# Optimization experiments

Measured on AMD Instinct MI355X. Metric: run time of the kernel, lower is better.

## Reference

```python
import jax, jax.numpy as jnp
import numpy as np

N = 10000
E = 160000
D_IN = 512
D_OUT = 512


def setup_inputs() -> dict:
    key = jax.random.key(0)
    k1, k2, k3, k4, k5 = jax.random.split(key, 5)
    x = jax.random.normal(k1, (N, D_IN), dtype=jnp.float32)
    edge_index = jax.random.randint(k2, (2, E), 0, N, dtype=jnp.int64)
    edge_attr = jax.random.uniform(k3, (E,), dtype=jnp.float32)
    W = jax.random.normal(k4, (D_IN, D_OUT), dtype=jnp.float32) * 0.05
    b = jax.random.normal(k5, (D_OUT,), dtype=jnp.float32) * 0.05
    return {"x": x, "edge_index": edge_index, "edge_attr": edge_attr, "W": W, "b": b}


def reference(x, edge_index, edge_attr, W, b):
    # PyG GCNConv with normalize=True, add_self_loops=True, edge_weight=edge_attr.
    n = x.shape[0]
    row, col = edge_index[0], edge_index[1]
    # Add self loops with weight 1.0 (fill_value=1.)
    loop = jnp.arange(n, dtype=edge_index.dtype)
    row_f = jnp.concatenate([row, loop])      # [E+N] source nodes
    col_f = jnp.concatenate([col, loop])      # [E+N] target nodes
    ew = jnp.concatenate([edge_attr, jnp.ones((n,), dtype=edge_attr.dtype)])
    # Symmetric normalization: deg computed over target index (col)
    deg = jax.ops.segment_sum(ew, col_f, num_segments=n)
    dinv = jnp.where(deg > 0, jax.lax.rsqrt(deg), 0.0)
    norm = dinv[row_f] * ew * dinv[col_f]     # [E+N]
    # Linear transform (no bias inside lin), then gather-scale-scatter
    h = x @ W                                  # [N, D_OUT]
    msg = h[row_f] * norm[:, None]             # [E+N, D_OUT]
    out = jax.ops.segment_sum(msg, col_f, num_segments=n)
    return out + b
```

## Files before the change

### kernel.cpp

```cpp
#include <hip/hip_runtime.h>

#define NN 10000
#define EE 160000
#define DD 512
#define CAP 128

typedef float floatx4 __attribute__((ext_vector_type(4)));
typedef short short8 __attribute__((ext_vector_type(8)));

#define AS3(p) ((__attribute__((address_space(3))) void*)(p))
#define AS1(p) ((const __attribute__((address_space(1))) void*)(p))

static __device__ __forceinline__ unsigned short f2bf(float f) {
    unsigned int u = __float_as_uint(f);
    unsigned int r = (u + 0x7fffu + ((u >> 16) & 1u)) >> 16;
    return (unsigned short)r;
}
static __device__ __forceinline__ unsigned int cvtpk(float a, float b) {
    unsigned int r;
    asm("v_cvt_pk_bf16_f32 %0, %1, %2" : "=v"(r) : "v"(a), "v"(b));
    return r;
}
static __device__ __forceinline__ float bflo(unsigned int u) {
    return __uint_as_float(u << 16);
}
static __device__ __forceinline__ float bfhi(unsigned int u) {
    return __uint_as_float(u & 0xffff0000u);
}


#define XB_BLOCKS 5000
#define WT_BLOCKS 256
#define ZERO_BLOCKS 20
#define EDGE_BLOCKS 625
#define GM_BLOCKS (157 * 4)

__global__ __launch_bounds__(256) void k_prep_xw(const float* __restrict__ x,
                                                 const float* __restrict__ W,
                                                 unsigned short* __restrict__ xb,
                                                 unsigned short* __restrict__ wtb,
                                                 uint4* __restrict__ zbase) {
    const int b = blockIdx.x;
    const int tid = threadIdx.x;
    if (b < XB_BLOCKS) {
        int gid = b * 256 + tid;
        float4 v = *(const float4*)&x[(size_t)gid * 4];
        *(uint2*)&xb[(size_t)gid * 4] = make_uint2(cvtpk(v.x, v.y), cvtpk(v.z, v.w));
    } else if (b < XB_BLOCKS + WT_BLOCKS) {
        __shared__ float T[32][33];
        int idx = b - XB_BLOCKS;
        int bi = idx & 15;
        int bj = idx >> 4;
        int r0 = tid >> 5;
        int cc = tid & 31;
        #pragma unroll
        for (int k = 0; k < 4; k++) {
            int r = r0 + k * 8;
            T[r][cc] = W[(size_t)(bi * 32 + r) * DD + bj * 32 + cc];
        }
        __syncthreads();
        #pragma unroll
        for (int k = 0; k < 4; k++) {
            int r = r0 + k * 8;
            wtb[(size_t)(bj * 32 + r) * DD + bi * 32 + cc] = f2bf(T[cc][r]);
        }
    } else {
        int idx = (b - XB_BLOCKS - WT_BLOCKS) * 256 + tid;
        zbase[idx] = make_uint4(0u, 0u, 0u, 0u);
    }
}


__global__ __launch_bounds__(256) void k_gemm_edge(const unsigned short* __restrict__ xb,
                                                   const unsigned short* __restrict__ wtb,
                                                   unsigned short* __restrict__ hb,
                                                   const int* __restrict__ row,
                                                   const int* __restrict__ col,
                                                   const float* __restrict__ ew,
                                                   float* __restrict__ deg,
                                                   int* __restrict__ cursor,
                                                   uint2* __restrict__ erw) {
    __shared__ unsigned short As[64 * 32];
    __shared__ unsigned short Bs[128 * 32];

    const int tid = threadIdx.x;

    if (blockIdx.x < EDGE_BLOCKS) {
        int e = blockIdx.x * 256 + tid;
        int r = row[e];
        int t = col[e];
        float w = ew[e];
        atomicAdd(&deg[t], w);
        int p = atomicAdd(&cursor[t], 1);
        if (p < CAP) erw[t * CAP + p] = make_uint2((unsigned int)r, __float_as_uint(w));
        return;
    }

    const int bid = blockIdx.x - EDGE_BLOCKS;
    const int wave = tid >> 6;
    const int lane = tid & 63;

    const int bm = (bid >> 2) * 64;
    const int bn = (bid & 3) * 128;

    const int wm = (wave >> 1) * 32;
    const int wn = (wave & 1) * 64;

    const int fm = lane & 15;
    const int kb = (lane >> 4) * 8;

    floatx4 acc[2][4];
    #pragma unroll
    for (int i = 0; i < 2; i++)
        #pragma unroll
        for (int j = 0; j < 4; j++)
            acc[i][j] = (floatx4){0.f, 0.f, 0.f, 0.f};

    const int srow = lane >> 2;
    const int scol = (lane & 3) * 8;

    for (int k0 = 0; k0 < DD; k0 += 32) {
        {
            int r = wave * 16 + srow;
            int gr = bm + r; if (gr > NN - 1) gr = NN - 1;
            __builtin_amdgcn_global_load_lds(AS1(xb + (size_t)gr * DD + k0 + scol),
                                             AS3(&As[wave * 512]), 16, 0, 0);
        }
        #pragma unroll
        for (int cc = 0; cc < 2; cc++) {
            int c = wave + cc * 4;
            int nr = bn + c * 16 + srow;
            __builtin_amdgcn_global_load_lds(AS1(wtb + (size_t)nr * DD + k0 + scol),
                                             AS3(&Bs[c * 512]), 16, 0, 0);
        }
        __syncthreads();

        short8 af[2], bfr[4];
        #pragma unroll
        for (int mi = 0; mi < 2; mi++)
            af[mi] = *(const short8*)&As[(wm + mi * 16 + fm) * 32 + kb];
        #pragma unroll
        for (int ni = 0; ni < 4; ni++)
            bfr[ni] = *(const short8*)&Bs[(wn + ni * 16 + fm) * 32 + kb];

        #pragma unroll
        for (int mi = 0; mi < 2; mi++)
            #pragma unroll
            for (int ni = 0; ni < 4; ni++)
                acc[mi][ni] = __builtin_amdgcn_mfma_f32_16x16x32_bf16(af[mi], bfr[ni], acc[mi][ni], 0, 0, 0);

        __syncthreads();
    }

    #pragma unroll
    for (int mi = 0; mi < 2; mi++) {
        #pragma unroll
        for (int ni = 0; ni < 4; ni++) {
            int colg = bn + wn + ni * 16 + (lane & 15);
            int rbase = bm + wm + mi * 16 + (lane >> 4) * 4;
            #pragma unroll
            for (int j = 0; j < 4; j++) {
                int rg = rbase + j;
                if (rg < NN) hb[(size_t)rg * DD + colg] = f2bf(acc[mi][ni][j]);
            }
        }
    }
}


#define EDGE_FMA(P, W) a0 += bflo(P) * W; a1 += bfhi(P) * W;

__global__ __launch_bounds__(128, 8) void k_aggregate(const int* __restrict__ cursor,
                                                      const uint2* __restrict__ erw,
                                                      const unsigned short* __restrict__ hb,
                                                      const float* __restrict__ deg,
                                                      const float* __restrict__ bias,
                                                      float* __restrict__ out) {
    const int h = threadIdx.x >> 6;
    const int t = threadIdx.x & 63;
    const int bid = blockIdx.x;
    const int q = bid & 3;
    const int i = (bid >> 2) * 2 + h;
    const int c = q * 128 + t * 2;

    __shared__ int   s_r[2][CAP];
    __shared__ float s_w[2][CAP];

    int cnt = cursor[i];
    if (cnt > CAP) cnt = CAP;
    const uint2* bkt = erw + (size_t)i * CAP;
    if (t < cnt) {
        uint2 p = bkt[t];
        int r = (int)p.x;
        s_r[h][t] = r << 9;
        s_w[h][t] = __uint_as_float(p.y) * rsqrtf(deg[r] + 1.0f);
    }
    if (t + 64 < cnt) {
        uint2 p = bkt[t + 64];
        int r = (int)p.x;
        s_r[h][t + 64] = r << 9;
        s_w[h][t + 64] = __uint_as_float(p.y) * rsqrtf(deg[r] + 1.0f);
    }

    float dv = rsqrtf(deg[i] + 1.0f);
    unsigned int hv = *(const unsigned int*)&hb[(size_t)i * DD + c];
    float2 bv = *(const float2*)&bias[c];

    __syncthreads();

    float a0 = 0.f, a1 = 0.f;

    int j = 0;
    for (; j + 8 <= cnt; j += 8) {
        unsigned int p0 = *(const unsigned int*)&hb[s_r[h][j    ] + c];
        unsigned int p1 = *(const unsigned int*)&hb[s_r[h][j + 1] + c];
        unsigned int p2 = *(const unsigned int*)&hb[s_r[h][j + 2] + c];
        unsigned int p3 = *(const unsigned int*)&hb[s_r[h][j + 3] + c];
        unsigned int p4 = *(const unsigned int*)&hb[s_r[h][j + 4] + c];
        unsigned int p5 = *(const unsigned int*)&hb[s_r[h][j + 5] + c];
        unsigned int p6 = *(const unsigned int*)&hb[s_r[h][j + 6] + c];
        unsigned int p7 = *(const unsigned int*)&hb[s_r[h][j + 7] + c];
        float w0 = s_w[h][j],     w1 = s_w[h][j + 1], w2 = s_w[h][j + 2], w3 = s_w[h][j + 3];
        float w4 = s_w[h][j + 4], w5 = s_w[h][j + 5], w6 = s_w[h][j + 6], w7 = s_w[h][j + 7];
        EDGE_FMA(p0, w0) EDGE_FMA(p1, w1) EDGE_FMA(p2, w2) EDGE_FMA(p3, w3)
        EDGE_FMA(p4, w4) EDGE_FMA(p5, w5) EDGE_FMA(p6, w6) EDGE_FMA(p7, w7)
    }
    for (; j + 4 <= cnt; j += 4) {
        unsigned int p0 = *(const unsigned int*)&hb[s_r[h][j    ] + c];
        unsigned int p1 = *(const unsigned int*)&hb[s_r[h][j + 1] + c];
        unsigned int p2 = *(const unsigned int*)&hb[s_r[h][j + 2] + c];
        unsigned int p3 = *(const unsigned int*)&hb[s_r[h][j + 3] + c];
        float w0 = s_w[h][j], w1 = s_w[h][j + 1], w2 = s_w[h][j + 2], w3 = s_w[h][j + 3];
        EDGE_FMA(p0, w0) EDGE_FMA(p1, w1) EDGE_FMA(p2, w2) EDGE_FMA(p3, w3)
    }
    for (; j < cnt; j++) {
        unsigned int p0 = *(const unsigned int*)&hb[s_r[h][j] + c];
        float w0 = s_w[h][j];
        EDGE_FMA(p0, w0)
    }

    float2 o;
    o.x = (a0 + bflo(hv) * dv) * dv + bv.x;
    o.y = (a1 + bfhi(hv) * dv) * dv + bv.y;
    *(float2*)&out[(size_t)i * DD + c] = o;
}

extern "C" void kernel_launch(void* const* d_in, const int* in_sizes, int n_in,
                              void* d_out, int out_size, void* d_ws, size_t ws_size,
                              hipStream_t stream) {
    const float* x  = (const float*)d_in[0];
    const int*   ei = (const int*)d_in[1];
    const float* ea = (const float*)d_in[2];
    const float* W  = (const float*)d_in[3];
    const float* b  = (const float*)d_in[4];
    float* out = (float*)d_out;

    char* ws = (char*)d_ws;
    unsigned short* hb   = (unsigned short*)ws;
    unsigned short* xb   = (unsigned short*)(ws + 10240000);
    unsigned short* wtb  = (unsigned short*)(ws + 20480000);
    float* deg    = (float*)(ws + 21004288);
    int*   cursor = (int*)  (ws + 21045248);
    uint2* erw    = (uint2*)(ws + 21086208);

    const int* row = ei;
    const int* col = ei + EE;

    k_prep_xw<<<XB_BLOCKS + WT_BLOCKS + ZERO_BLOCKS, 256, 0, stream>>>(x, W, xb, wtb, (uint4*)deg);

    k_gemm_edge<<<EDGE_BLOCKS + GM_BLOCKS, 256, 0, stream>>>(xb, wtb, hb, row, col, ea,
                                                             deg, cursor, erw);

    k_aggregate<<<NN * 2, 128, 0, stream>>>(cursor, erw, hb, deg, b, out);
}
```

Measured before the change: 128.5 us.

## Fuse three kernels into one persistent cooperative kernel with grid syncs

```diff
diff --git a/kernel.cpp b/kernel.cpp
--- a/kernel.cpp
+++ b/kernel.cpp
@@ -1,4 +1,5 @@
 #include <hip/hip_runtime.h>
+#include <hip/hip_cooperative_groups.h>
 
 #define NN 10000
 #define EE 160000
@@ -28,12 +29,193 @@
     return __uint_as_float(u & 0xffff0000u);
 }
 
-
-#define XB_BLOCKS 5000
-#define WT_BLOCKS 256
-#define ZERO_BLOCKS 20
-#define EDGE_BLOCKS 625
-#define GM_BLOCKS (157 * 4)
+#define XB_TASKS 5000
+#define WT_TASKS 256
+#define ZERO_TASKS 20
+#define PREP_TASKS (XB_TASKS + WT_TASKS + ZERO_TASKS)
+#define GEMM_TASKS 628
+#define EDGE_TASKS 625
+#define PHASEB_TASKS (GEMM_TASKS + EDGE_TASKS)
+#define AGG_TASKS (NN * 2)
+
+__global__ __launch_bounds__(256) void k_fused(const float* __restrict__ x,
+                                               const float* __restrict__ W,
+                                               const int* __restrict__ row,
+                                               const int* __restrict__ col,
+                                               const float* __restrict__ ew,
+                                               unsigned short* __restrict__ xb,
+                                               unsigned short* __restrict__ wtb,
+                                               unsigned short* __restrict__ hb,
+                                               float* __restrict__ deg,
+                                               int* __restrict__ cursor,
+                                               uint2* __restrict__ erw,
+                                               const float* __restrict__ bias,
+                                               float* __restrict__ out) {
+    __shared__ unsigned short As[64 * 32];
+    __shared__ unsigned short Bs[128 * 32];
+    __shared__ float T[32][33];
+
+    const int tid = threadIdx.x;
+    const int nb = gridDim.x;
+    const int wave = tid >> 6;
+    const int lane = tid & 63;
+
+    for (int task = blockIdx.x; task < PREP_TASKS; task += nb) {
+        if (task < XB_TASKS) {
+            int gid = task * 256 + tid;
+            float4 v = *(const float4*)&x[(size_t)gid * 4];
+            *(uint2*)&xb[(size_t)gid * 4] = make_uint2(cvtpk(v.x, v.y), cvtpk(v.z, v.w));
+        } else if (task < XB_TASKS + WT_TASKS) {
+            int idx = task - XB_TASKS;
+            int bi = idx & 15;
+            int bj = idx >> 4;
+            int r0 = tid >> 5;
+            int cc = tid & 31;
+            #pragma unroll
+            for (int k = 0; k < 4; k++) {
+                int r = r0 + k * 8;
+                T[r][cc] = W[(size_t)(bi * 32 + r) * DD + bj * 32 + cc];
+            }
+            __syncthreads();
+            #pragma unroll
+            for (int k = 0; k < 4; k++) {
+                int r = r0 + k * 8;
+                wtb[(size_t)(bj * 32 + r) * DD + bi * 32 + cc] = f2bf(T[cc][r]);
+            }
+            __syncthreads();
+        } else {
+            int idx = (task - XB_TASKS - WT_TASKS) * 256 + tid;
+            ((uint4*)deg)[idx] = make_uint4(0u, 0u, 0u, 0u);
+        }
+    }
+
+    __threadfence();
+    cooperative_groups::this_grid().sync();
+
+    for (int task = blockIdx.x; task < PHASEB_TASKS; task += nb) {
+        if (task >= GEMM_TASKS) {
+            int e = (task - GEMM_TASKS) * 256 + tid;
+            int r = row[e];
+            int t = col[e];
+            float w = ew[e];
+            atomicAdd(&deg[t], w);
+            int p = atomicAdd(&cursor[t], 1);
+            if (p < CAP) erw[t * CAP + p] = make_uint2((unsigned int)r, __float_as_uint(w));
+        } else {
+            const int bid = task;
+            const int bm = (bid >> 2) * 64;
+            const int bn = (bid & 3) * 128;
+            const int wm = (wave >> 1) * 32;
+            const int wn = (wave & 1) * 64;
+            const int fm = lane & 15;
+            const int kb = (lane >> 4) * 8;
+            const int srow = lane >> 2;
+            const int scol = (lane & 3) * 8;
+
+            floatx4 acc[2][4];
+            #pragma unroll
+            for (int i = 0; i < 2; i++)
+                #pragma unroll
+                for (int j = 0; j < 4; j++)
+                    acc[i][j] = (floatx4){0.f, 0.f, 0.f, 0.f};
+
+            int gr = bm + wave * 16 + srow; if (gr > NN - 1) gr = NN - 1;
+
+            for (int k0 = 0; k0 < DD; k0 += 32) {
+                __builtin_amdgcn_global_load_lds(AS1(xb + (size_t)gr * DD + k0 + scol),
+                                                 AS3(&As[wave * 512]), 16, 0, 0);
+                #pragma unroll
+                for (int cc = 0; cc < 2; cc++) {
+                    int c = wave + cc * 4;
+                    int nr = bn + c * 16 + srow;
+                    __builtin_amdgcn_global_load_lds(AS1(wtb + (size_t)nr * DD + k0 + scol),
+                                                     AS3(&Bs[c * 512]), 16, 0, 0);
+                }
+                __syncthreads();
+
+                short8 af[2], bfr[4];
+                #pragma unroll
+                for (int mi = 0; mi < 2; mi++)
+                    af[mi] = *(const short8*)&As[(wm + mi * 16 + fm) * 32 + kb];
+                #pragma unroll
+                for (int ni = 0; ni < 4; ni++)
+                    bfr[ni] = *(const short8*)&Bs[(wn + ni * 16 + fm) * 32 + kb];
+
+                #pragma unroll
+                for (int mi = 0; mi < 2; mi++)
+                    #pragma unroll
+                    for (int ni = 0; ni < 4; ni++)
+                        acc[mi][ni] = __builtin_amdgcn_mfma_f32_16x16x32_bf16(af[mi], bfr[ni], acc[mi][ni], 0, 0, 0);
+
+                __syncthreads();
+            }
+
+            #pragma unroll
+            for (int mi = 0; mi < 2; mi++) {
+                #pragma unroll
+                for (int ni = 0; ni < 4; ni++) {
+                    int colg = bn + wn + ni * 16 + (lane & 15);
+                    int rbase = bm + wm + mi * 16 + (lane >> 4) * 4;
+                    #pragma unroll
+                    for (int j = 0; j < 4; j++) {
+                        int rg = rbase + j;
+                        if (rg < NN) hb[(size_t)rg * DD + colg] = f2bf(acc[mi][ni][j]);
+                    }
+                }
+            }
+        }
+    }
+
+    __threadfence();
+    cooperative_groups::this_grid().sync();
+
+    const int wgid = blockIdx.x * 4 + wave;
+    const int wstride = nb * 4;
+    for (int t = wgid; t < AGG_TASKS; t += wstride) {
+        const int i = t >> 1;
+        const int c = (t & 1) * 256 + lane * 4;
+        int cnt = cursor[i];
+        if (cnt > CAP) cnt = CAP;
+        const uint2* bkt = erw + (size_t)i * CAP;
+
+        uint2 e0 = make_uint2((unsigned int)i, 0u);
+        uint2 e1 = make_uint2((unsigned int)i, 0u);
+        if (lane < cnt)      e0 = bkt[lane];
+        if (lane + 64 < cnt) e1 = bkt[lane + 64];
+        float wt0 = (lane < cnt)      ? __uint_as_float(e0.y) * rsqrtf(deg[e0.x] + 1.0f) : 0.0f;
+        float wt1 = (lane + 64 < cnt) ? __uint_as_float(e1.y) * rsqrtf(deg[e1.x] + 1.0f) : 0.0f;
+        int rb0 = (int)e0.x << 9;
+        int rb1 = (int)e1.x << 9;
+
+        float dvv = rsqrtf(deg[i] + 1.0f);
+        uint2 hv = *(const uint2*)&hb[(size_t)i * DD + c];
+        float4 bv = *(const float4*)&bias[c];
+
+        float a0 = 0.f, a1 = 0.f, a2 = 0.f, a3 = 0.f;
+        int cr = (cnt + 7) & ~7;
+        for (int j = 0; j < cr; j += 8) {
+            int rbs   = (j < 64) ? rb0 : rb1;
+            float wss = (j < 64) ? wt0 : wt1;
+            int base = j & 63;
+            #pragma unroll
+            for (int u = 0; u < 8; u++) {
+                int rbase = __shfl(rbs, base + u, 64);
+                float wq  = __shfl(wss, base + u, 64);
+                uint2 p = *(const uint2*)&hb[rbase + c];
+                a0 += bflo(p.x) * wq; a1 += bfhi(p.x) * wq;
+                a2 += bflo(p.y) * wq; a3 += bfhi(p.y) * wq;
+            }
+        }
+
+        float4 o;
+        o.x = (a0 + bflo(hv.x) * dvv) * dvv + bv.x;
+        o.y = (a1 + bfhi(hv.x) * dvv) * dvv + bv.y;
+        o.z = (a2 + bflo(hv.y) * dvv) * dvv + bv.z;
+        o.w = (a3 + bfhi(hv.y) * dvv) * dvv + bv.w;
+        *(float4*)&out[(size_t)i * DD + c] = o;
+    }
+}
+
 
 __global__ __launch_bounds__(256) void k_prep_xw(const float* __restrict__ x,
                                                  const float* __restrict__ W,
@@ -42,17 +224,15 @@
                                                  uint4* __restrict__ zbase) {
     const int b = blockIdx.x;
     const int tid = threadIdx.x;
-    if (b < XB_BLOCKS) {
+    if (b < XB_TASKS) {
         int gid = b * 256 + tid;
         float4 v = *(const float4*)&x[(size_t)gid * 4];
         *(uint2*)&xb[(size_t)gid * 4] = make_uint2(cvtpk(v.x, v.y), cvtpk(v.z, v.w));
-    } else if (b < XB_BLOCKS + WT_BLOCKS) {
+    } else if (b < XB_TASKS + WT_TASKS) {
         __shared__ float T[32][33];
-        int idx = b - XB_BLOCKS;
-        int bi = idx & 15;
-        int bj = idx >> 4;
-        int r0 = tid >> 5;
-        int cc = tid & 31;
+        int idx = b - XB_TASKS;
+        int bi = idx & 15, bj = idx >> 4;
+        int r0 = tid >> 5, cc = tid & 31;
         #pragma unroll
         for (int k = 0; k < 4; k++) {
             int r = r0 + k * 8;
@@ -65,11 +245,10 @@
             wtb[(size_t)(bj * 32 + r) * DD + bi * 32 + cc] = f2bf(T[cc][r]);
         }
     } else {
-        int idx = (b - XB_BLOCKS - WT_BLOCKS) * 256 + tid;
+        int idx = (b - XB_TASKS - WT_TASKS) * 256 + tid;
         zbase[idx] = make_uint4(0u, 0u, 0u, 0u);
     }
 }
-
 
 __global__ __launch_bounds__(256) void k_gemm_edge(const unsigned short* __restrict__ xb,
                                                    const unsigned short* __restrict__ wtb,
@@ -82,10 +261,9 @@
                                                    uint2* __restrict__ erw) {
     __shared__ unsigned short As[64 * 32];
     __shared__ unsigned short Bs[128 * 32];
-
     const int tid = threadIdx.x;
 
-    if (blockIdx.x < EDGE_BLOCKS) {
+    if (blockIdx.x < EDGE_TASKS) {
         int e = blockIdx.x * 256 + tid;
         int r = row[e];
         int t = col[e];
@@ -96,16 +274,13 @@
         return;
     }
 
-    const int bid = blockIdx.x - EDGE_BLOCKS;
+    const int bid = blockIdx.x - EDGE_TASKS;
     const int wave = tid >> 6;
     const int lane = tid & 63;
-
     const int bm = (bid >> 2) * 64;
     const int bn = (bid & 3) * 128;
-
     const int wm = (wave >> 1) * 32;
     const int wn = (wave & 1) * 64;
-
     const int fm = lane & 15;
     const int kb = (lane >> 4) * 8;
 
@@ -166,7 +341,6 @@
         }
     }
 }
-
 
 #define EDGE_FMA(P, W) a0 += bflo(P) * W; a1 += bfhi(P) * W;
 
@@ -209,7 +383,6 @@
     __syncthreads();
 
     float a0 = 0.f, a1 = 0.f;
-
     int j = 0;
     for (; j + 8 <= cnt; j += 8) {
         unsigned int p0 = *(const unsigned int*)&hb[s_r[h][j    ] + c];
@@ -225,14 +398,6 @@
         EDGE_FMA(p0, w0) EDGE_FMA(p1, w1) EDGE_FMA(p2, w2) EDGE_FMA(p3, w3)
         EDGE_FMA(p4, w4) EDGE_FMA(p5, w5) EDGE_FMA(p6, w6) EDGE_FMA(p7, w7)
     }
-    for (; j + 4 <= cnt; j += 4) {
-        unsigned int p0 = *(const unsigned int*)&hb[s_r[h][j    ] + c];
-        unsigned int p1 = *(const unsigned int*)&hb[s_r[h][j + 1] + c];
-        unsigned int p2 = *(const unsigned int*)&hb[s_r[h][j + 2] + c];
-        unsigned int p3 = *(const unsigned int*)&hb[s_r[h][j + 3] + c];
-        float w0 = s_w[h][j], w1 = s_w[h][j + 1], w2 = s_w[h][j + 2], w3 = s_w[h][j + 3];
-        EDGE_FMA(p0, w0) EDGE_FMA(p1, w1) EDGE_FMA(p2, w2) EDGE_FMA(p3, w3)
-    }
     for (; j < cnt; j++) {
         unsigned int p0 = *(const unsigned int*)&hb[s_r[h][j] + c];
         float w0 = s_w[h][j];
@@ -244,6 +409,7 @@
     o.y = (a1 + bfhi(hv) * dv) * dv + bv.y;
     *(float2*)&out[(size_t)i * DD + c] = o;
 }
+
 
 extern "C" void kernel_launch(void* const* d_in, const int* in_sizes, int n_in,
                               void* d_out, int out_size, void* d_ws, size_t ws_size,
@@ -266,10 +432,27 @@
     const int* row = ei;
     const int* col = ei + EE;
 
-    k_prep_xw<<<XB_BLOCKS + WT_BLOCKS + ZERO_BLOCKS, 256, 0, stream>>>(x, W, xb, wtb, (uint4*)deg);
-
-    k_gemm_edge<<<EDGE_BLOCKS + GM_BLOCKS, 256, 0, stream>>>(xb, wtb, hb, row, col, ea,
-                                                             deg, cursor, erw);
-
-    k_aggregate<<<NN * 2, 128, 0, stream>>>(cursor, erw, hb, deg, b, out);
-}
+    static int coop_grid = 0;
+    if (coop_grid == 0) {
+        int per_cu = 0;
+        hipOccupancyMaxActiveBlocksPerMultiprocessor(&per_cu, k_fused, 256, 0);
+        if (per_cu < 1) per_cu = 1;
+        if (per_cu > 8) per_cu = 8;
+        coop_grid = per_cu * 256;
+    }
+
+    void* args[] = { (void*)&x, (void*)&W, (void*)&row, (void*)&col, (void*)&ea,
+                     (void*)&xb, (void*)&wtb, (void*)&hb,
+                     (void*)&deg, (void*)&cursor, (void*)&erw,
+                     (void*)&b, (void*)&out };
+
+    hipError_t err = hipLaunchCooperativeKernel((const void*)k_fused,
+                                                dim3(coop_grid), dim3(256),
+                                                args, 0, stream);
+    if (err != hipSuccess) {
+        k_prep_xw<<<XB_TASKS + WT_TASKS + ZERO_TASKS, 256, 0, stream>>>(x, W, xb, wtb, (uint4*)deg);
+        k_gemm_edge<<<EDGE_TASKS + GEMM_TASKS, 256, 0, stream>>>(xb, wtb, hb, row, col, ea,
+                                                                 deg, cursor, erw);
+        k_aggregate<<<NN * 2, 128, 0, stream>>>(cursor, erw, hb, deg, b, out);
+    }
+}
```

Measured after the change: 376.4 us. +193.0%, slower.
